# Performance work log

Measured on AMD Instinct MI355X. Metric: run time of the kernel, lower is better.

## Reference

```python
import jax, jax.numpy as jnp
import numpy as np

K = 32            # config.k: active latents per token (batch top-k)
THRESHOLD_LR = 0.01
B, S, F = 8, 256, 16384


def setup_inputs() -> dict:
    key = jax.random.key(0)
    k1, k2 = jax.random.split(key)
    x = jax.random.normal(k1, (B, S, F), dtype=jnp.float32)
    token_mask = jax.random.randint(k2, (B, S), 0, 2, dtype=jnp.int32)
    threshold = jnp.zeros((), dtype=jnp.float32)  # persistent EMA buffer, init 0.0
    return {"x": x, "token_mask": token_mask, "threshold": threshold}


def reference(x, token_mask, threshold):
    # Training path of BatchTopKActivationFunction.forward
    b, s, f = x.shape
    num_tokens = b * s
    k_total = K * num_tokens
    neg_min = jnp.finfo(x.dtype).min
    # mask out tokens: x[~token_mask] = finfo.min (so they never enter top-k)
    xm = jnp.where(token_mask.astype(bool)[:, :, None], x, neg_min)
    flat = xm.reshape(-1)                       # [b*s*f]
    vals, idx = jax.lax.top_k(flat, k_total)    # global top-k over flattened tensor
    # scatter relu'd top-k values back into a zero tensor
    result = jnp.zeros_like(flat).at[idx].set(jax.nn.relu(vals)).reshape(b, s, f)
    # EMA threshold update: min of strictly-positive selected values
    pos = vals > 0
    min_pos = jnp.min(jnp.where(pos, vals, jnp.inf))
    new_threshold = jnp.where(
        jnp.any(pos),
        (1.0 - THRESHOLD_LR) * threshold + THRESHOLD_LR * min_pos,
        threshold,
    )
    return result, new_threshold
```

## Files before the change

kernel.cpp:

```cpp
#include <hip/hip_runtime.h>

#define N_ELEMS  33554432
#define N4       8388608
#define N_TOKENS 2048
#define F4       4096
#define K_TOTAL  65536u
#define NBINS    4096

#define C_NG       4096
#define C_N2       4101
#define N_CTR_END  4160

#define GLIST_OFF  8192u
#define CAPG       4194304u
#define LIST2_OFF  (GLIST_OFF + 2u*CAPG)
#define CAP2       4096u
#define FB1_OFF    16777216u
#define CAPF       2097152u
#define FB2_OFF    (FB1_OFF + 2u*CAPF)

#define GBUF 1024

__device__ __forceinline__ unsigned keyOf(float f) {
    unsigned b = __float_as_uint(f);
    return b ^ ((unsigned)((int)b >> 31) | 0x80000000u);
}
__device__ __forceinline__ float valOf(unsigned u) {
    unsigned b = (u & 0x80000000u) ? (u ^ 0x80000000u) : ~u;
    return __uint_as_float(b);
}
__device__ __forceinline__ unsigned umaxu(unsigned a, unsigned b) { return a > b ? a : b; }

__global__ void k_init(unsigned* __restrict__ ws) {
    int t = blockIdx.x * 256 + threadIdx.x;
    if (t < N_CTR_END) ws[t] = 0u;
}

__global__ __launch_bounds__(512) void k_hist(const float4* __restrict__ x,
                                              const int* __restrict__ mask,
                                              unsigned* __restrict__ ws,
                                              float4* __restrict__ out) {
    __shared__ unsigned lh[NBINS];
    __shared__ uint2 sbuf[GBUF];
    __shared__ unsigned s_cnt, s_base;
    const int tok = blockIdx.x;
    const int tid = threadIdx.x;
    float4* ot = out + (size_t)tok * F4;
    const float4 z = make_float4(0.f, 0.f, 0.f, 0.f);
    if (!mask[tok]) {
        for (int j = tid; j < F4; j += 512) ot[j] = z;
        return;
    }
    for (int b = tid; b < NBINS; b += 512) lh[b] = 0u;
    if (tid == 0) s_cnt = 0u;
    __syncthreads();
    uint2* glist = (uint2*)(ws + GLIST_OFF);
    const float4* xt = x + (size_t)tok * F4;
    const unsigned baseIdx = (unsigned)tok * 16384u;
    #pragma unroll
    for (int half = 0; half < 2; ++half) {
        const int j0 = tid + half * 2048;
        float4 v0 = xt[j0];
        float4 v1 = xt[j0 + 512];
        float4 v2 = xt[j0 + 1024];
        float4 v3 = xt[j0 + 1536];
        ot[j0] = z; ot[j0 + 512] = z; ot[j0 + 1024] = z; ot[j0 + 1536] = z;
        float fv[16] = {v0.x, v0.y, v0.z, v0.w, v1.x, v1.y, v1.z, v1.w,
                        v2.x, v2.y, v2.z, v2.w, v3.x, v3.y, v3.z, v3.w};
        #pragma unroll
        for (int c = 0; c < 16; ++c) {
            float f = fv[c];
            if (f >= 2.0f) {
                unsigned u = keyOf(f);
                unsigned bin = (u - 0xC0000000u) >> 12;
                if (bin > 4095u) bin = 4095u;
                atomicAdd(&lh[bin], 1u);
                unsigned slot = atomicAdd(&s_cnt, 1u);
                unsigned j = (unsigned)(j0 + (c >> 2) * 512);
                uint2 e = make_uint2(u, baseIdx + j * 4u + (unsigned)(c & 3));
                if (slot < GBUF) sbuf[slot] = e;
                else { unsigned g = atomicAdd(&ws[C_NG], 1u); if (g < CAPG) glist[g] = e; }
            }
        }
    }
    __syncthreads();
    for (int b = tid; b < NBINS; b += 512) {
        unsigned c = lh[b];
        if (c) atomicAdd(&ws[b], c);
    }
    unsigned cnt = s_cnt; if (cnt > GBUF) cnt = GBUF;
    if (tid == 0) s_base = atomicAdd(&ws[C_NG], cnt);
    __syncthreads();
    for (unsigned j = tid; j < cnt; j += 512) {
        unsigned p = s_base + j;
        if (p < CAPG) glist[p] = sbuf[j];
    }
}

__global__ __launch_bounds__(256) void k_scatter(unsigned* __restrict__ ws,
                                                 float* __restrict__ out) {
    __shared__ unsigned sc[256];
    __shared__ unsigned s_b1, s_ka, s_found;
    const int t = threadIdx.x;
    unsigned vv[16];
    unsigned s = 0u;
    #pragma unroll
    for (int j = 0; j < 16; ++j) { vv[j] = ws[t * 16 + j]; s += vv[j]; }
    if (t == 0) { s_found = 0u; s_b1 = 0u; s_ka = 0u; }
    sc[t] = s;
    __syncthreads();
    for (int off = 1; off < 256; off <<= 1) {
        unsigned a = sc[t];
        unsigned b = (t + off < 256) ? sc[t + off] : 0u;
        __syncthreads();
        sc[t] = a + b;
        __syncthreads();
    }
    unsigned run = (t < 255) ? sc[t + 1] : 0u;
    #pragma unroll
    for (int j = 15; j >= 0; --j) {
        unsigned prev = run; run += vv[j];
        if (run >= K_TOTAL && prev < K_TOTAL) {
            s_b1 = (unsigned)(t * 16 + j); s_ka = prev; s_found = 1u;
        }
    }
    __syncthreads();
    const unsigned total = sc[0];
    unsigned ngRaw = ws[C_NG];
    if ((s_found == 0u) || (total < K_TOTAL) || (s_b1 == 4095u) || (ngRaw > CAPG))
        return;
    const unsigned candTh = 0xC0000000u + (s_b1 << 12);
    const unsigned winTh  = candTh + 0x1000u;
    unsigned ng = ngRaw;
    uint2* glist = (uint2*)(ws + GLIST_OFF);
    uint2* list2 = (uint2*)(ws + LIST2_OFF);
    const unsigned stride = gridDim.x * 256u;
    for (unsigned i = blockIdx.x * 256u + (unsigned)t; i < ng; i += stride) {
        uint2 e = glist[i];
        if (e.x >= winTh) out[e.y] = valOf(e.x);
        else if (e.x >= candTh) {
            unsigned g = atomicAdd(&ws[C_N2], 1u);
            if (g < CAP2) list2[g] = e;
        }
    }
}

__global__ __launch_bounds__(1024) void k_tail(const float4* __restrict__ x,
                                               const int* __restrict__ mask,
                                               unsigned* __restrict__ ws,
                                               float* __restrict__ out,
                                               const float* __restrict__ thr) {
    __shared__ __align__(16) unsigned smem[9216];
    __shared__ unsigned s_b1, s_ka, s_found, s_fb, s_need, s_n2;
    __shared__ unsigned sB1, sKA, sMode, sNegmin, sB2, sNeed, sCnt;
    const int t = threadIdx.x;

    {
        unsigned* sc = smem;
        unsigned vv[4];
        unsigned s = 0u;
        #pragma unroll
        for (int j = 0; j < 4; ++j) { vv[j] = ws[t * 4 + j]; s += vv[j]; }
        if (t == 0) { s_found = 0u; s_b1 = 0u; s_ka = 0u; }
        sc[t] = s;
        __syncthreads();
        for (int off = 1; off < 1024; off <<= 1) {
            unsigned a = sc[t];
            unsigned b = (t + off < 1024) ? sc[t + off] : 0u;
            __syncthreads();
            sc[t] = a + b;
            __syncthreads();
        }
        unsigned run = (t < 1023) ? sc[t + 1] : 0u;
        #pragma unroll
        for (int j = 3; j >= 0; --j) {
            unsigned prev = run; run += vv[j];
            if (run >= K_TOTAL && prev < K_TOTAL) {
                s_b1 = (unsigned)(t * 4 + j); s_ka = prev; s_found = 1u;
            }
        }
        __syncthreads();
        if (t == 0) {
            unsigned total = sc[0];
            unsigned ng = ws[C_NG];
            unsigned n2v = ws[C_N2];
            unsigned fb = (s_found == 0u) || (total < K_TOTAL) || (s_b1 == 4095u) ||
                          (ng > CAPG) || (n2v > CAP2);
            s_fb = fb; s_need = K_TOTAL - s_ka; s_n2 = n2v;
        }
        __syncthreads();
    }

    if (!s_fb) {
        uint2* ent = (uint2*)smem;
        unsigned* red = smem + 8192;
        const unsigned n2 = s_n2;
        const unsigned need = s_need;
        uint2* list2 = (uint2*)(ws + LIST2_OFF);
        for (unsigned i = (unsigned)t; i < n2; i += 1024u) ent[i] = list2[i];
        __syncthreads();
        unsigned minSel = 0xFFFFFFFFu;
        for (unsigned i = (unsigned)t; i < n2; i += 1024u) {
            uint2 e = ent[i];
            unsigned rank = 0u;
            for (unsigned j = 0; j < n2; ++j) {
                uint2 o = ent[j];
                rank += (o.x > e.x || (o.x == e.x && o.y < e.y)) ? 1u : 0u;
            }
            if (rank < need) {
                out[e.y] = valOf(e.x);
                if (e.x < minSel) minSel = e.x;
            }
        }
        red[t] = minSel;
        __syncthreads();
        for (int off = 512; off > 0; off >>= 1) {
            if (t < off) red[t] = red[t] < red[t + off] ? red[t] : red[t + off];
            __syncthreads();
        }
        if (t == 0) {
            out[N_ELEMS] = 0.99f * thr[0] + 0.01f * valOf(red[0]);
        }
        return;
    }

    unsigned* lh = smem;
    unsigned* sred = smem + 4096;
    for (int b = t; b < NBINS; b += 1024) lh[b] = 0u;
    if (t == 0) sCnt = 0u;
    __syncthreads();
    unsigned negmin = 0u;
    for (int tok = 0; tok < N_TOKENS; ++tok) {
        if (!mask[tok]) continue;
        const float4* xt = x + (size_t)tok * F4;
        for (int j = t; j < F4; j += 1024) {
            float4 v = xt[j];
            float fv[4] = {v.x, v.y, v.z, v.w};
            #pragma unroll
            for (int c = 0; c < 4; ++c) {
                float f = fv[c];
                unsigned u = keyOf(f);
                atomicAdd(&lh[u >> 20], 1u);
                if (f > 0.0f) negmin = umaxu(negmin, ~u);
            }
        }
    }
    __syncthreads();
    sred[t] = negmin; __syncthreads();
    for (int off = 512; off > 0; off >>= 1) {
        if (t < off) sred[t] = umaxu(sred[t], sred[t + off]);
        __syncthreads();
    }
    if (t == 0) {
        sNegmin = sred[0];
        unsigned tot = 0u;
        for (int b = 0; b < NBINS; ++b) tot += lh[b];
        if (tot <= K_TOTAL) sMode = 1u;
        else {
            sMode = 0u;
            unsigned run = 0u, prev = 0u; int b1 = 0;
            for (int b = NBINS - 1; b >= 0; --b) {
                prev = run; run += lh[b];
                if (run >= K_TOTAL && prev < K_TOTAL) { b1 = b; break; }
            }
            sB1 = (unsigned)b1; sKA = prev;
        }
        sCnt = 0u;
    }
    __syncthreads();
    if (sMode == 1u) {
        for (int tok = 0; tok < N_TOKENS; ++tok) {
            if (!mask[tok]) continue;
            const float4* xt = x + (size_t)tok * F4;
            float* ot = out + (size_t)tok * 16384;
            for (int j = t; j < F4; j += 1024) {
                float4 v = xt[j];
                ot[j * 4 + 0] = fmaxf(v.x, 0.f); ot[j * 4 + 1] = fmaxf(v.y, 0.f);
                ot[j * 4 + 2] = fmaxf(v.z, 0.f); ot[j * 4 + 3] = fmaxf(v.w, 0.f);
            }
        }
        if (t == 0) {
            float th = thr[0], newt = th;
            if (sNegmin) newt = 0.99f * th + 0.01f * valOf(~sNegmin);
            out[N_ELEMS] = newt;
        }
        return;
    }
    const unsigned B1c = sB1;
    uint2* fb1 = (uint2*)(ws + FB1_OFF);
    for (int tok = 0; tok < N_TOKENS; ++tok) {
        if (!mask[tok]) continue;
        const float4* xt = x + (size_t)tok * F4;
        const unsigned baseIdx = (unsigned)tok * 16384u;
        for (int j = t; j < F4; j += 1024) {
            float4 v = xt[j];
            float fv[4] = {v.x, v.y, v.z, v.w};
            #pragma unroll
            for (int c = 0; c < 4; ++c) {
                float f = fv[c];
                unsigned u = keyOf(f);
                unsigned p = u >> 20;
                unsigned idx = baseIdx + (unsigned)j * 4u + (unsigned)c;
                if (p > B1c) out[idx] = fmaxf(f, 0.f);
                else if (p == B1c) {
                    unsigned g = atomicAdd(&sCnt, 1u);
                    if (g < CAPF) fb1[g] = make_uint2(u, idx);
                }
            }
        }
    }
    __syncthreads();
    unsigned n1 = sCnt > CAPF ? CAPF : sCnt;
    __syncthreads();
    if (t < 256) lh[t] = 0u;
    if (t == 0) sCnt = 0u;
    __syncthreads();
    for (unsigned i = t; i < n1; i += 1024)
        atomicAdd(&lh[(fb1[i].x >> 12) & 255u], 1u);
    __syncthreads();
    if (t == 0) {
        unsigned run = sKA, prev = sKA; int b2 = 0;
        for (int b = 255; b >= 0; --b) {
            prev = run; run += lh[b];
            if (run >= K_TOTAL) { b2 = b; break; }
        }
        sB2 = (unsigned)b2; sNeed = K_TOTAL - prev;
    }
    __syncthreads();
    const unsigned B2 = sB2, need = sNeed;
    uint2* fb2 = (uint2*)(ws + FB2_OFF);
    for (unsigned i = t; i < n1; i += 1024) {
        uint2 e = fb1[i];
        unsigned bb = (e.x >> 12) & 255u;
        if (bb > B2) out[e.y] = fmaxf(valOf(e.x), 0.f);
        else if (bb == B2) {
            unsigned g = atomicAdd(&sCnt, 1u);
            if (g < CAPF) fb2[g] = e;
        }
    }
    __syncthreads();
    unsigned n2 = sCnt > CAPF ? CAPF : sCnt;
    unsigned minSel = 0xFFFFFFFFu;
    for (unsigned i = t; i < n2; i += 1024) {
        uint2 e = fb2[i];
        unsigned rank = 0u;
        for (unsigned jj = 0; jj < n2; ++jj) {
            uint2 o = fb2[jj];
            rank += (o.x > e.x || (o.x == e.x && o.y < e.y)) ? 1u : 0u;
        }
        if (rank < need) { out[e.y] = fmaxf(valOf(e.x), 0.f); if (e.x < minSel) minSel = e.x; }
    }
    __syncthreads();
    sred[t] = minSel; __syncthreads();
    for (int off = 512; off > 0; off >>= 1) {
        if (t < off) sred[t] = sred[t] < sred[t + off] ? sred[t] : sred[t + off];
        __syncthreads();
    }
    if (t == 0) {
        float th = thr[0], newt = th;
        unsigned vku = sred[0];
        if (vku != 0xFFFFFFFFu) {
            float vk = valOf(vku);
            float minpos; int any;
            if (vk > 0.f) { minpos = vk; any = 1; }
            else { any = (sNegmin != 0u); minpos = any ? valOf(~sNegmin) : 0.f; }
            if (any) newt = 0.99f * th + 0.01f * minpos;
        }
        out[N_ELEMS] = newt;
    }
}

extern "C" void kernel_launch(void* const* d_in, const int* in_sizes, int n_in,
                              void* d_out, int out_size, void* d_ws, size_t ws_size,
                              hipStream_t stream) {
    const float4* x  = (const float4*)d_in[0];
    const int* mask  = (const int*)d_in[1];
    const float* thr = (const float*)d_in[2];
    float* out       = (float*)d_out;
    unsigned* ws     = (unsigned*)d_ws;

    k_init    <<<17, 256, 0, stream>>>(ws);
    k_hist    <<<N_TOKENS, 512, 0, stream>>>(x, mask, ws, (float4*)out);
    k_scatter <<<512, 256, 0, stream>>>(ws, out);
    k_tail    <<<1, 1024, 0, stream>>>(x, mask, ws, out, thr);
}
```

Before: 267.0 us.

## Move histogram out of streaming pass into separate candidate-list histogram kernel

The per-token streaming kernel no longer builds a 4096-bin shared histogram or flushes it to global memory with atomics. A new 32-block kernel builds that histogram from the compacted candidate list, and its last block computes the threshold bin once and stores the thresholds and need count in the workspace. The scatter and tail kernels then read these values instead of each repeating the prefix scan. This takes shared-memory atomics and the 2048-block global flush off the bandwidth-bound pass, at the cost of an extra launch, a second read of the candidate keys, and a last-block-done handshake.

```diff
diff --git a/kernel.cpp b/kernel.cpp
--- a/kernel.cpp
+++ b/kernel.cpp
@@ -8,7 +8,12 @@
 #define NBINS    4096
 
 #define C_NG       4096
+#define C_WINTH    4097
+#define C_CANDTH   4098
+#define C_NEED     4099
+#define C_FB       4100
 #define C_N2       4101
+#define C_DONE     4102
 #define N_CTR_END  4160
 
 #define GLIST_OFF  8192u
@@ -20,6 +25,7 @@
 #define FB2_OFF    (FB1_OFF + 2u*CAPF)
 
 #define GBUF 1024
+#define GH_BLOCKS 32
 
 __device__ __forceinline__ unsigned keyOf(float f) {
     unsigned b = __float_as_uint(f);
@@ -36,11 +42,10 @@
     if (t < N_CTR_END) ws[t] = 0u;
 }
 
-__global__ __launch_bounds__(512) void k_hist(const float4* __restrict__ x,
-                                              const int* __restrict__ mask,
-                                              unsigned* __restrict__ ws,
-                                              float4* __restrict__ out) {
-    __shared__ unsigned lh[NBINS];
+__global__ __launch_bounds__(512) void k_stream(const float4* __restrict__ x,
+                                                const int* __restrict__ mask,
+                                                unsigned* __restrict__ ws,
+                                                float4* __restrict__ out) {
     __shared__ uint2 sbuf[GBUF];
     __shared__ unsigned s_cnt, s_base;
     const int tok = blockIdx.x;
@@ -51,7 +56,6 @@
         for (int j = tid; j < F4; j += 512) ot[j] = z;
         return;
     }
-    for (int b = tid; b < NBINS; b += 512) lh[b] = 0u;
     if (tid == 0) s_cnt = 0u;
     __syncthreads();
     uint2* glist = (uint2*)(ws + GLIST_OFF);
@@ -72,9 +76,6 @@
             float f = fv[c];
             if (f >= 2.0f) {
                 unsigned u = keyOf(f);
-                unsigned bin = (u - 0xC0000000u) >> 12;
-                if (bin > 4095u) bin = 4095u;
-                atomicAdd(&lh[bin], 1u);
                 unsigned slot = atomicAdd(&s_cnt, 1u);
                 unsigned j = (unsigned)(j0 + (c >> 2) * 512);
                 uint2 e = make_uint2(u, baseIdx + j * 4u + (unsigned)(c & 3));
@@ -84,10 +85,6 @@
         }
     }
     __syncthreads();
-    for (int b = tid; b < NBINS; b += 512) {
-        unsigned c = lh[b];
-        if (c) atomicAdd(&ws[b], c);
-    }
     unsigned cnt = s_cnt; if (cnt > GBUF) cnt = GBUF;
     if (tid == 0) s_base = atomicAdd(&ws[C_NG], cnt);
     __syncthreads();
@@ -97,45 +94,83 @@
     }
 }
 
+__global__ __launch_bounds__(1024) void k_ghist(unsigned* __restrict__ ws) {
+    __shared__ unsigned lh[NBINS];
+    __shared__ unsigned s_last, s_b1, s_ka, s_found;
+    const int t = threadIdx.x;
+    for (int b = t; b < NBINS; b += 1024) lh[b] = 0u;
+    if (t == 0) s_last = 0u;
+    __syncthreads();
+    const unsigned ngRaw = ws[C_NG];
+    unsigned ng = ngRaw > CAPG ? CAPG : ngRaw;
+    const uint2* glist = (const uint2*)(ws + GLIST_OFF);
+    for (unsigned i = blockIdx.x * 1024u + (unsigned)t; i < ng; i += GH_BLOCKS * 1024u) {
+        unsigned u = glist[i].x;
+        unsigned bin = (u - 0xC0000000u) >> 12;
+        if (bin > 4095u) bin = 4095u;
+        atomicAdd(&lh[bin], 1u);
+    }
+    __syncthreads();
+    for (int b = t; b < NBINS; b += 1024) {
+        unsigned c = lh[b];
+        if (c) atomicAdd(&ws[b], c);
+    }
+    __syncthreads();
+    if (t == 0) {
+        __threadfence();
+        unsigned done = atomicAdd(&ws[C_DONE], 1u) + 1u;
+        if (done == GH_BLOCKS) s_last = 1u;
+    }
+    __syncthreads();
+    if (!s_last) return;
+    unsigned vv[4]; unsigned s = 0u;
+    #pragma unroll
+    for (int j = 0; j < 4; ++j) {
+        vv[j] = __hip_atomic_load(&ws[t * 4 + j], __ATOMIC_RELAXED, __HIP_MEMORY_SCOPE_AGENT);
+        s += vv[j];
+    }
+    unsigned* sc = lh;
+    if (t == 0) s_found = 0u;
+    sc[t] = s;
+    __syncthreads();
+    for (int off = 1; off < 1024; off <<= 1) {
+        unsigned a = sc[t];
+        unsigned b2 = (t + off < 1024) ? sc[t + off] : 0u;
+        __syncthreads();
+        sc[t] = a + b2;
+        __syncthreads();
+    }
+    unsigned run = (t < 1023) ? sc[t + 1] : 0u;
+    #pragma unroll
+    for (int j = 3; j >= 0; --j) {
+        unsigned prev = run; run += vv[j];
+        if (run >= K_TOTAL && prev < K_TOTAL) {
+            s_b1 = (unsigned)(t * 4 + j); s_ka = prev; s_found = 1u;
+        }
+    }
+    __syncthreads();
+    if (t == 0) {
+        unsigned total = sc[0];
+        unsigned fb = (s_found == 0u) || (total < K_TOTAL) || (s_b1 == 4095u) || (ngRaw > CAPG);
+        ws[C_FB] = fb ? 1u : 0u;
+        if (!fb) {
+            unsigned candTh = 0xC0000000u + (s_b1 << 12);
+            ws[C_CANDTH] = candTh;
+            ws[C_WINTH]  = candTh + 0x1000u;
+            ws[C_NEED]   = K_TOTAL - s_ka;
+        }
+    }
+}
+
 __global__ __launch_bounds__(256) void k_scatter(unsigned* __restrict__ ws,
                                                  float* __restrict__ out) {
-    __shared__ unsigned sc[256];
-    __shared__ unsigned s_b1, s_ka, s_found;
-    const int t = threadIdx.x;
-    unsigned vv[16];
-    unsigned s = 0u;
-    #pragma unroll
-    for (int j = 0; j < 16; ++j) { vv[j] = ws[t * 16 + j]; s += vv[j]; }
-    if (t == 0) { s_found = 0u; s_b1 = 0u; s_ka = 0u; }
-    sc[t] = s;
-    __syncthreads();
-    for (int off = 1; off < 256; off <<= 1) {
-        unsigned a = sc[t];
-        unsigned b = (t + off < 256) ? sc[t + off] : 0u;
-        __syncthreads();
-        sc[t] = a + b;
-        __syncthreads();
-    }
-    unsigned run = (t < 255) ? sc[t + 1] : 0u;
-    #pragma unroll
-    for (int j = 15; j >= 0; --j) {
-        unsigned prev = run; run += vv[j];
-        if (run >= K_TOTAL && prev < K_TOTAL) {
-            s_b1 = (unsigned)(t * 16 + j); s_ka = prev; s_found = 1u;
-        }
-    }
-    __syncthreads();
-    const unsigned total = sc[0];
-    unsigned ngRaw = ws[C_NG];
-    if ((s_found == 0u) || (total < K_TOTAL) || (s_b1 == 4095u) || (ngRaw > CAPG))
-        return;
-    const unsigned candTh = 0xC0000000u + (s_b1 << 12);
-    const unsigned winTh  = candTh + 0x1000u;
-    unsigned ng = ngRaw;
+    if (ws[C_FB]) return;
+    const unsigned winTh = ws[C_WINTH], candTh = ws[C_CANDTH];
+    unsigned ng = ws[C_NG]; if (ng > CAPG) ng = CAPG;
     uint2* glist = (uint2*)(ws + GLIST_OFF);
     uint2* list2 = (uint2*)(ws + LIST2_OFF);
     const unsigned stride = gridDim.x * 256u;
-    for (unsigned i = blockIdx.x * 256u + (unsigned)t; i < ng; i += stride) {
+    for (unsigned i = blockIdx.x * 256u + (unsigned)threadIdx.x; i < ng; i += stride) {
         uint2 e = glist[i];
         if (e.x >= winTh) out[e.y] = valOf(e.x);
         else if (e.x >= candTh) {
@@ -151,51 +186,16 @@
                                                float* __restrict__ out,
                                                const float* __restrict__ thr) {
     __shared__ __align__(16) unsigned smem[9216];
-    __shared__ unsigned s_b1, s_ka, s_found, s_fb, s_need, s_n2;
     __shared__ unsigned sB1, sKA, sMode, sNegmin, sB2, sNeed, sCnt;
     const int t = threadIdx.x;
-
-    {
-        unsigned* sc = smem;
-        unsigned vv[4];
-        unsigned s = 0u;
-        #pragma unroll
-        for (int j = 0; j < 4; ++j) { vv[j] = ws[t * 4 + j]; s += vv[j]; }
-        if (t == 0) { s_found = 0u; s_b1 = 0u; s_ka = 0u; }
-        sc[t] = s;
-        __syncthreads();
-        for (int off = 1; off < 1024; off <<= 1) {
-            unsigned a = sc[t];
-            unsigned b = (t + off < 1024) ? sc[t + off] : 0u;
-            __syncthreads();
-            sc[t] = a + b;
-            __syncthreads();
-        }
-        unsigned run = (t < 1023) ? sc[t + 1] : 0u;
-        #pragma unroll
-        for (int j = 3; j >= 0; --j) {
-            unsigned prev = run; run += vv[j];
-            if (run >= K_TOTAL && prev < K_TOTAL) {
-                s_b1 = (unsigned)(t * 4 + j); s_ka = prev; s_found = 1u;
-            }
-        }
-        __syncthreads();
-        if (t == 0) {
-            unsigned total = sc[0];
-            unsigned ng = ws[C_NG];
-            unsigned n2v = ws[C_N2];
-            unsigned fb = (s_found == 0u) || (total < K_TOTAL) || (s_b1 == 4095u) ||
-                          (ng > CAPG) || (n2v > CAP2);
-            s_fb = fb; s_need = K_TOTAL - s_ka; s_n2 = n2v;
-        }
-        __syncthreads();
-    }
-
-    if (!s_fb) {
+    const unsigned rawn2 = ws[C_N2];
+    const unsigned fb = ws[C_FB] | (rawn2 > CAP2 ? 1u : 0u);
+
+    if (!fb) {
         uint2* ent = (uint2*)smem;
         unsigned* red = smem + 8192;
-        const unsigned n2 = s_n2;
-        const unsigned need = s_need;
+        const unsigned n2 = rawn2;
+        const unsigned need = ws[C_NEED];
         uint2* list2 = (uint2*)(ws + LIST2_OFF);
         for (unsigned i = (unsigned)t; i < n2; i += 1024u) ent[i] = list2[i];
         __syncthreads();
@@ -380,7 +380,8 @@
     unsigned* ws     = (unsigned*)d_ws;
 
     k_init    <<<17, 256, 0, stream>>>(ws);
-    k_hist    <<<N_TOKENS, 512, 0, stream>>>(x, mask, ws, (float4*)out);
-    k_scatter <<<512, 256, 0, stream>>>(ws, out);
+    k_stream  <<<N_TOKENS, 512, 0, stream>>>(x, mask, ws, (float4*)out);
+    k_ghist   <<<GH_BLOCKS, 1024, 0, stream>>>(ws);
+    k_scatter <<<256, 256, 0, stream>>>(ws, out);
     k_tail    <<<1, 1024, 0, stream>>>(x, mask, ws, out, thr);
 }
```

New measurement: 272.3 us. About the same (+2.0%).
